# Optimization experiments

Measured on AMD Instinct MI355X. Metric: run time of the kernel, lower is better.

The kernel has to match this reference:

```python
import jax, jax.numpy as jnp
import numpy as np


def setup_inputs() -> dict:
    key = jax.random.key(0)
    k1, k2, k3 = jax.random.split(key, 3)
    N, K, d, d_out = 100000, 32, 64, 64
    x = jax.random.normal(k1, (N, d), dtype=jnp.float32)
    edge_index = jax.random.randint(k2, (N, K), 0, N, dtype=jnp.int64)
    W = jax.random.normal(k3, (2 * d, d_out), dtype=jnp.float32) * (1.0 / np.sqrt(2 * d))
    b = jnp.zeros((d_out,), dtype=jnp.float32)
    return {"x": x, "edge_index": edge_index, "W": W, "b": b}


def reference(x, edge_index, W, b):
    # x: [N, d], edge_index: [N, K] dense neighbor indices
    x_j = x[edge_index]                                  # [N, K, d] gather
    # concat([x_i, x_j - x_i]) then max over K. The x_i half is constant over K,
    # so its max is x itself; max of the diff half computed directly (same math,
    # avoids materializing the [N, K, 2d] concat).
    diff_max = jnp.max(x_j - x[:, None, :], axis=1)      # [N, d]
    h = jnp.concatenate([x, diff_max], axis=-1)          # [N, 2d]
    return h @ W + b                                     # [N, d_out]
```

## Files before the change

### kernel.cpp

```cpp
#include <hip/hip_runtime.h>
#include <hip/hip_bf16.h>
#include <cstdint>


typedef __attribute__((ext_vector_type(8))) short short8;
typedef __attribute__((ext_vector_type(4))) float f4;
typedef __attribute__((ext_vector_type(8))) unsigned short u16x8;
typedef __attribute__((ext_vector_type(4))) unsigned int u32x4;

#define TILE 16
#define ROWS 168

__device__ __forceinline__ unsigned short f2bf(float f) {
  unsigned int u = __builtin_bit_cast(unsigned int, f);
  u += 0x7fffu + ((u >> 16) & 1u);
  return (unsigned short)(u >> 16);
}
__device__ __forceinline__ unsigned int pack2(float a, float b) {
  return (unsigned int)f2bf(a) | ((unsigned int)f2bf(b) << 16);
}
__device__ __forceinline__ float bflo(unsigned int u) {
  return __builtin_bit_cast(float, u << 16);
}
__device__ __forceinline__ float bfhi(unsigned int u) {
  return __builtin_bit_cast(float, u & 0xffff0000u);
}
__device__ __forceinline__ unsigned int key2(unsigned int u) {
  unsigned int s = u & 0x80008000u;
  unsigned int m = (s >> 15) * 0x7fffu;
  return u ^ (0x80008000u | m);
}
__device__ __forceinline__ unsigned int unkey2(unsigned int k) {
  unsigned int s = k & 0x80008000u;
  unsigned int m = ((s >> 15) ^ 0x00010001u) * 0x7fffu;
  return k ^ (0x80008000u | m);
}
__device__ __forceinline__ u16x8 pmax8(u16x8 a, u16x8 b) {
  return __builtin_elementwise_max(a, b);
}

__global__ __launch_bounds__(256)
void convert_kernel(const float* __restrict__ x, unsigned int* __restrict__ xbf,
                    const float* __restrict__ W, unsigned short* __restrict__ wf,
                    int n8, int nxb) {
  if ((int)blockIdx.x < nxb) {
    int i = blockIdx.x * 256 + threadIdx.x;
    if (i >= n8) return;
    const f4* p = (const f4*)x + (size_t)i * 2;
    f4 a = __builtin_nontemporal_load(p);
    f4 b = __builtin_nontemporal_load(p + 1);
    u32x4 w;
    w.x = key2(pack2(a.x, a.y)); w.y = key2(pack2(a.z, a.w));
    w.z = key2(pack2(b.x, b.y)); w.w = key2(pack2(b.z, b.w));
    ((u32x4*)xbf)[i] = w;
  } else {
    #pragma unroll
    for (int q = 0; q < 4; ++q) {
      int idx = threadIdx.x * 4 + q;
      int wv = idx >> 8, ks = (idx >> 6) & 3, l = idx & 63;
      int c = l & 15, g = l >> 4;
      short8 v;
      #pragma unroll
      for (int j = 0; j < 8; ++j)
        v[j] = (short)f2bf(W[(ks * 32 + g * 8 + j) * 64 + wv * 16 + c]);
      *(short8*)(wf + (size_t)idx * 8) = v;
    }
  }
}

__global__ __launch_bounds__(256, 4)
void mrconv3_kernel(const unsigned int* __restrict__ xbf,
                    const unsigned short* __restrict__ wf,
                    const int* __restrict__ ei,
                    const float* __restrict__ bias,
                    float* __restrict__ out,
                    int n_tiles)
{
  __shared__ __align__(16) unsigned short hs[TILE * ROWS];
  __shared__ __align__(16) int eis[TILE * 32];
  __shared__ __align__(16) float otile[TILE * 64];

  const int tid  = threadIdx.x;
  const int wv   = tid >> 6;
  const int lane = tid & 63;
  const int c = lane & 15;
  const int g = lane >> 4;
  const int t2 = lane >> 4;
  const int h  = (lane >> 3) & 1;
  const int e  = lane & 7;

  const int node0 = blockIdx.x * TILE;
  const int t = wv * 4 + t2;

  {
    long long ev = __builtin_nontemporal_load(
        (const long long*)ei + (size_t)node0 * 16 + tid);
    const int ts = tid >> 4, qs = tid & 15;
    eis[ts * 32 + qs]      = (int)ev;
    eis[ts * 32 + 16 + qs] = (int)(ev >> 32);
  }
  __syncthreads();

  const char* __restrict__ xb = (const char*)xbf;
  const unsigned eoff = (unsigned)e * 16u;
  const u16x8 xrk = *(const u16x8*)(xb + ((unsigned)(node0 + t) * 128u + eoff));

  const int4* ip = (const int4*)&eis[(t * 2 + h) * 16];
  const int4 i0 = ip[0], i1 = ip[1], i2 = ip[2], i3 = ip[3];
  const int jj[16] = {i0.x, i0.y, i0.z, i0.w, i1.x, i1.y, i1.z, i1.w,
                      i2.x, i2.y, i2.z, i2.w, i3.x, i3.y, i3.z, i3.w};
  u16x8 r[16];
  #pragma unroll
  for (int q = 0; q < 16; ++q) {
    const unsigned vo = ((unsigned)jj[q] << 7) + eoff;
    asm volatile("global_load_dwordx4 %0, %1, %2"
                 : "=v"(r[q]) : "v"(vo), "s"(xbf));
  }
  asm volatile("s_waitcnt vmcnt(0)" ::: "memory");
  __builtin_amdgcn_sched_barrier(0);

  u16x8 ka = pmax8(r[0], r[1]);
  u16x8 kb = pmax8(r[2], r[3]);
  #pragma unroll
  for (int q = 4; q < 16; q += 4) {
    ka = pmax8(ka, pmax8(r[q],     r[q + 1]));
    kb = pmax8(kb, pmax8(r[q + 2], r[q + 3]));
  }
  u16x8 km = pmax8(ka, kb);

  u32x4 k4 = __builtin_bit_cast(u32x4, km);
  u32x4 s4;
  s4.x = (unsigned)__shfl_xor((int)k4.x, 8);
  s4.y = (unsigned)__shfl_xor((int)k4.y, 8);
  s4.z = (unsigned)__shfl_xor((int)k4.z, 8);
  s4.w = (unsigned)__shfl_xor((int)k4.w, 8);
  km = pmax8(km, __builtin_bit_cast(u16x8, s4));
  k4 = __builtin_bit_cast(u32x4, km);

  const u32x4 xr4 = __builtin_bit_cast(u32x4, xrk);
  u32x4 xw;
  xw.x = unkey2(xr4.x); xw.y = unkey2(xr4.y);
  xw.z = unkey2(xr4.z); xw.w = unkey2(xr4.w);

  if (h == 0) {
    const unsigned m0 = unkey2(k4.x), m1 = unkey2(k4.y);
    const unsigned m2 = unkey2(k4.z), m3 = unkey2(k4.w);
    u32x4 w;
    w.x = pack2(bflo(m0) - bflo(xw.x), bfhi(m0) - bfhi(xw.x));
    w.y = pack2(bflo(m1) - bflo(xw.y), bfhi(m1) - bfhi(xw.y));
    w.z = pack2(bflo(m2) - bflo(xw.z), bfhi(m2) - bfhi(xw.z));
    w.w = pack2(bflo(m3) - bflo(xw.w), bfhi(m3) - bfhi(xw.w));
    *(u32x4*)(hs + t * ROWS + 64 + e * 8) = w;
  } else {
    *(u32x4*)(hs + t * ROWS + e * 8) = xw;
  }

  short8 bfrag[4];
  #pragma unroll
  for (int ks = 0; ks < 4; ++ks)
    bfrag[ks] = *(const short8*)(wf + (size_t)((wv * 4 + ks) * 64 + lane) * 8);
  __syncthreads();

  f4 acc = {0.f, 0.f, 0.f, 0.f};
  #pragma unroll
  for (int ks = 0; ks < 4; ++ks) {
    short8 a = *(const short8*)(hs + c * ROWS + ks * 32 + g * 8);
    acc = __builtin_amdgcn_mfma_f32_16x16x32_bf16(a, bfrag[ks], acc, 0, 0, 0);
  }

  const float bb = bias[wv * 16 + c];
  #pragma unroll
  for (int j = 0; j < 4; ++j)
    otile[(g * 4 + j) * 64 + wv * 16 + c] = acc[j] + bb;
  __syncthreads();
  __builtin_nontemporal_store(*(const f4*)&otile[tid * 4],
                              (f4*)(out + (size_t)node0 * 64) + tid);
}

#define FWPB 4
#define FROWS 160
__global__ __launch_bounds__(256, 4)
void mrconv_fp32_kernel(const float* __restrict__ x,
                        const int* __restrict__ ei,
                        const float* __restrict__ W,
                        const float* __restrict__ bias,
                        float* __restrict__ out,
                        int n_tiles)
{
  __shared__ __align__(16) unsigned short hsf[FWPB][TILE * FROWS];
  const int wave = threadIdx.x >> 6;
  const int lane = threadIdx.x & 63;
  const int c = lane & 15;
  const int g = lane >> 4;

  short8 bfrag[4][4];
  #pragma unroll
  for (int ks = 0; ks < 4; ++ks) {
    #pragma unroll
    for (int nt = 0; nt < 4; ++nt) {
      short8 v;
      #pragma unroll
      for (int j = 0; j < 8; ++j) {
        int k = ks * 32 + g * 8 + j;
        v[j] = (short)f2bf(W[k * 64 + nt * 16 + c]);
      }
      bfrag[ks][nt] = v;
    }
  }

  const int tile = blockIdx.x * FWPB + wave;
  if (tile >= n_tiles) return;
  const int node0 = tile * TILE;
  unsigned short* hrow = &hsf[wave][0];

  #pragma unroll 2
  for (int t = 0; t < TILE; ++t) {
    const int n = node0 + t;
    const f4 xi = *(const f4*)(x + (size_t)n * 64 + 4 * c);
    f4 m = { -3.4e38f, -3.4e38f, -3.4e38f, -3.4e38f };
    #pragma unroll
    for (int it = 0; it < 8; ++it) {
      const int j = ei[(size_t)n * 32 + it * 4 + g];
      const f4 xj = *(const f4*)(x + (size_t)j * 64 + 4 * c);
      m.x = fmaxf(m.x, xj.x - xi.x);
      m.y = fmaxf(m.y, xj.y - xi.y);
      m.z = fmaxf(m.z, xj.z - xi.z);
      m.w = fmaxf(m.w, xj.w - xi.w);
    }
    m.x = fmaxf(m.x, __shfl_xor(m.x, 16));
    m.y = fmaxf(m.y, __shfl_xor(m.y, 16));
    m.z = fmaxf(m.z, __shfl_xor(m.z, 16));
    m.w = fmaxf(m.w, __shfl_xor(m.w, 16));
    m.x = fmaxf(m.x, __shfl_xor(m.x, 32));
    m.y = fmaxf(m.y, __shfl_xor(m.y, 32));
    m.z = fmaxf(m.z, __shfl_xor(m.z, 32));
    m.w = fmaxf(m.w, __shfl_xor(m.w, 32));
    if (g == 0) {
      ushort4 p;
      p.x = f2bf(xi.x); p.y = f2bf(xi.y); p.z = f2bf(xi.z); p.w = f2bf(xi.w);
      *(ushort4*)(hrow + t * FROWS + 4 * c) = p;
    } else if (g == 1) {
      ushort4 p;
      p.x = f2bf(m.x); p.y = f2bf(m.y); p.z = f2bf(m.z); p.w = f2bf(m.w);
      *(ushort4*)(hrow + t * FROWS + 64 + 4 * c) = p;
    }
  }
  __asm__ volatile("s_waitcnt lgkmcnt(0)" ::: "memory");

  f4 acc[4] = {{0.f,0.f,0.f,0.f},{0.f,0.f,0.f,0.f},{0.f,0.f,0.f,0.f},{0.f,0.f,0.f,0.f}};
  #pragma unroll
  for (int ks = 0; ks < 4; ++ks) {
    short8 a = *(const short8*)(hrow + c * FROWS + ks * 32 + g * 8);
    #pragma unroll
    for (int nt = 0; nt < 4; ++nt)
      acc[nt] = __builtin_amdgcn_mfma_f32_16x16x32_bf16(a, bfrag[ks][nt], acc[nt], 0, 0, 0);
  }
  const int rbase = node0 + g * 4;
  #pragma unroll
  for (int nt = 0; nt < 4; ++nt) {
    const float bb = bias[nt * 16 + c];
    #pragma unroll
    for (int j = 0; j < 4; ++j)
      out[(size_t)(rbase + j) * 64 + nt * 16 + c] = acc[nt][j] + bb;
  }
}

extern "C" void kernel_launch(void* const* d_in, const int* in_sizes, int n_in,
                              void* d_out, int out_size, void* d_ws, size_t ws_size,
                              hipStream_t stream) {
  const float* x  = (const float*)d_in[0];
  const int*   ei = (const int*)d_in[1];
  const float* W  = (const float*)d_in[2];
  const float* b  = (const float*)d_in[3];
  float* out = (float*)d_out;

  const int N = in_sizes[0] / 64;
  const int n_tiles = N / TILE;

  const size_t xbf_bytes = (size_t)N * 64 * 2;
  const size_t wf_bytes  = 1024 * 16;
  if (ws_size >= xbf_bytes + wf_bytes) {
    unsigned int*   xbf = (unsigned int*)d_ws;
    unsigned short* wf  = (unsigned short*)((char*)d_ws + xbf_bytes);
    const int n8  = N * 64 / 8;
    const int nxb = (n8 + 255) / 256;
    hipLaunchKernelGGL(convert_kernel, dim3(nxb + 1), dim3(256), 0, stream,
                       x, xbf, W, wf, n8, nxb);
    hipLaunchKernelGGL(mrconv3_kernel, dim3(n_tiles), dim3(256), 0, stream,
                       xbf, wf, ei, b, out, n_tiles);
  } else {
    const int blocks = (n_tiles + FWPB - 1) / FWPB;
    hipLaunchKernelGGL(mrconv_fp32_kernel, dim3(blocks), dim3(256), 0, stream,
                       x, ei, W, b, out, n_tiles);
  }
}
```

Before: 132.6 us.

## Stage neighbor gathers through LDS with double-buffered direct global-to-LDS loads

Replaces the 16 register-destined gather loads per lane with global_load_lds transfers into a per-wave double-buffered LDS staging area. The max reduction over one batch now overlaps with the in-flight loads of the next. It also reorders the edge-index layout in shared memory, hoists the weight fragment loads before the first barrier, and writes outputs straight to global instead of through an LDS tile and extra barrier. In exchange it uses more LDS per block, which may limit occupancy, and adds LDS round trips plus fine-grained waitcnt sequencing.

```diff
diff --git a/kernel.cpp b/kernel.cpp
--- a/kernel.cpp
+++ b/kernel.cpp
@@ -38,6 +38,18 @@
 __device__ __forceinline__ u16x8 pmax8(u16x8 a, u16x8 b) {
   return __builtin_elementwise_max(a, b);
 }
+__device__ __forceinline__ void gl16(const void* g, void* l) {
+  __builtin_amdgcn_global_load_lds(
+      (const __attribute__((address_space(1))) void*)g,
+      (__attribute__((address_space(3))) void*)l, 16, 0, 0);
+}
+
+#define WAITV4 do { asm volatile("s_waitcnt vmcnt(4)" ::: "memory"); \
+                    __builtin_amdgcn_sched_barrier(0); } while (0)
+#define WAITV0 do { asm volatile("s_waitcnt vmcnt(0)" ::: "memory"); \
+                    __builtin_amdgcn_sched_barrier(0); } while (0)
+#define WAITL0 do { asm volatile("s_waitcnt lgkmcnt(0)" ::: "memory"); \
+                    __builtin_amdgcn_sched_barrier(0); } while (0)
 
 __global__ __launch_bounds__(256)
 void convert_kernel(const float* __restrict__ x, unsigned int* __restrict__ xbf,
@@ -69,25 +81,26 @@
 }
 
 __global__ __launch_bounds__(256, 4)
-void mrconv3_kernel(const unsigned int* __restrict__ xbf,
+void mrconv4_kernel(const unsigned int* __restrict__ xbf,
                     const unsigned short* __restrict__ wf,
                     const int* __restrict__ ei,
                     const float* __restrict__ bias,
                     float* __restrict__ out,
                     int n_tiles)
 {
+  __shared__ __align__(16) unsigned short stg[4][2][2048];
+  __shared__ __align__(16) int eis3[512];
   __shared__ __align__(16) unsigned short hs[TILE * ROWS];
-  __shared__ __align__(16) int eis[TILE * 32];
-  __shared__ __align__(16) float otile[TILE * 64];
 
   const int tid  = threadIdx.x;
   const int wv   = tid >> 6;
   const int lane = tid & 63;
-  const int c = lane & 15;
-  const int g = lane >> 4;
+  const int c  = lane & 15;
+  const int g  = lane >> 4;
   const int t2 = lane >> 4;
-  const int h  = (lane >> 3) & 1;
+  const int rr = (lane >> 3) & 1;
   const int e  = lane & 7;
+  const int s  = lane >> 3;
 
   const int node0 = blockIdx.x * TILE;
   const int t = wv * 4 + t2;
@@ -96,36 +109,65 @@
     long long ev = __builtin_nontemporal_load(
         (const long long*)ei + (size_t)node0 * 16 + tid);
     const int ts = tid >> 4, qs = tid & 15;
-    eis[ts * 32 + qs]      = (int)ev;
-    eis[ts * 32 + 16 + qs] = (int)(ev >> 32);
-  }
+    const int k0 = qs * 2, k1 = qs * 2 + 1;
+    eis3[((k0 & 7) * 16 + ts) * 4 + (k0 >> 3)] = (int)ev;
+    eis3[((k1 & 7) * 16 + ts) * 4 + (k1 >> 3)] = (int)(ev >> 32);
+  }
+
+  const char* __restrict__ xb = (const char*)xbf;
+  const unsigned co = (unsigned)e * 16u;
+  const u16x8 xrk = *(const u16x8*)(xb + (size_t)((unsigned)(node0 + t) * 128u + co));
+  short8 bfrag[4];
+  #pragma unroll
+  for (int ks = 0; ks < 4; ++ks)
+    bfrag[ks] = *(const short8*)(wf + (size_t)((wv * 4 + ks) * 64 + lane) * 8);
   __syncthreads();
 
-  const char* __restrict__ xb = (const char*)xbf;
-  const unsigned eoff = (unsigned)e * 16u;
-  const u16x8 xrk = *(const u16x8*)(xb + ((unsigned)(node0 + t) * 128u + eoff));
-
-  const int4* ip = (const int4*)&eis[(t * 2 + h) * 16];
-  const int4 i0 = ip[0], i1 = ip[1], i2 = ip[2], i3 = ip[3];
-  const int jj[16] = {i0.x, i0.y, i0.z, i0.w, i1.x, i1.y, i1.z, i1.w,
-                      i2.x, i2.y, i2.z, i2.w, i3.x, i3.y, i3.z, i3.w};
-  u16x8 r[16];
-  #pragma unroll
-  for (int q = 0; q < 16; ++q) {
-    const unsigned vo = ((unsigned)jj[q] << 7) + eoff;
-    asm volatile("global_load_dwordx4 %0, %1, %2"
-                 : "=v"(r[q]) : "v"(vo), "s"(xbf));
-  }
-  asm volatile("s_waitcnt vmcnt(0)" ::: "memory");
-  __builtin_amdgcn_sched_barrier(0);
-
-  u16x8 ka = pmax8(r[0], r[1]);
-  u16x8 kb = pmax8(r[2], r[3]);
-  #pragma unroll
-  for (int q = 4; q < 16; q += 4) {
-    ka = pmax8(ka, pmax8(r[q],     r[q + 1]));
-    kb = pmax8(kb, pmax8(r[q + 2], r[q + 3]));
-  }
+  const int4 q0 = *(const int4*)&eis3[(s * 16 + wv * 4 + 0) * 4];
+  const int4 q1 = *(const int4*)&eis3[(s * 16 + wv * 4 + 1) * 4];
+  const int4 q2 = *(const int4*)&eis3[(s * 16 + wv * 4 + 2) * 4];
+  const int4 q3 = *(const int4*)&eis3[(s * 16 + wv * 4 + 3) * 4];
+
+  unsigned short* const sw0 = &stg[wv][0][0];
+  unsigned short* const sw1 = &stg[wv][1][0];
+
+#define ISS(I0, I1, I2, I3, SW)                                   \
+  gl16(xb + ((unsigned)(I0) * 128u + co), (SW));                  \
+  gl16(xb + ((unsigned)(I1) * 128u + co), (SW) + 512);            \
+  gl16(xb + ((unsigned)(I2) * 128u + co), (SW) + 1024);           \
+  gl16(xb + ((unsigned)(I3) * 128u + co), (SW) + 1536)
+
+  const unsigned rbase = (unsigned)t2 * 512 + (unsigned)rr * 256 + (unsigned)e * 8;
+
+  u16x8 ka, kb;
+#define RED_INIT(SW) {                                            \
+    const u16x8 v0 = *(const u16x8*)((SW) + rbase);               \
+    const u16x8 v1 = *(const u16x8*)((SW) + rbase + 64);          \
+    const u16x8 v2 = *(const u16x8*)((SW) + rbase + 128);         \
+    const u16x8 v3 = *(const u16x8*)((SW) + rbase + 192);         \
+    ka = pmax8(v0, v2); kb = pmax8(v1, v3); }
+#define RED_ACC(SW) {                                             \
+    const u16x8 v0 = *(const u16x8*)((SW) + rbase);               \
+    const u16x8 v1 = *(const u16x8*)((SW) + rbase + 64);          \
+    const u16x8 v2 = *(const u16x8*)((SW) + rbase + 128);         \
+    const u16x8 v3 = *(const u16x8*)((SW) + rbase + 192);         \
+    ka = pmax8(ka, pmax8(v0, v2)); kb = pmax8(kb, pmax8(v1, v3)); }
+
+  ISS(q0.x, q1.x, q2.x, q3.x, sw0);
+  ISS(q0.y, q1.y, q2.y, q3.y, sw1);
+  WAITV4;
+  RED_INIT(sw0);
+  WAITL0;
+  ISS(q0.z, q1.z, q2.z, q3.z, sw0);
+  WAITV4;
+  RED_ACC(sw1);
+  WAITL0;
+  ISS(q0.w, q1.w, q2.w, q3.w, sw1);
+  WAITV4;
+  RED_ACC(sw0);
+  WAITV0;
+  RED_ACC(sw1);
+
   u16x8 km = pmax8(ka, kb);
 
   u32x4 k4 = __builtin_bit_cast(u32x4, km);
@@ -142,7 +184,7 @@
   xw.x = unkey2(xr4.x); xw.y = unkey2(xr4.y);
   xw.z = unkey2(xr4.z); xw.w = unkey2(xr4.w);
 
-  if (h == 0) {
+  if (rr == 0) {
     const unsigned m0 = unkey2(k4.x), m1 = unkey2(k4.y);
     const unsigned m2 = unkey2(k4.z), m3 = unkey2(k4.w);
     u32x4 w;
@@ -154,11 +196,6 @@
   } else {
     *(u32x4*)(hs + t * ROWS + e * 8) = xw;
   }
-
-  short8 bfrag[4];
-  #pragma unroll
-  for (int ks = 0; ks < 4; ++ks)
-    bfrag[ks] = *(const short8*)(wf + (size_t)((wv * 4 + ks) * 64 + lane) * 8);
   __syncthreads();
 
   f4 acc = {0.f, 0.f, 0.f, 0.f};
@@ -171,10 +208,11 @@
   const float bb = bias[wv * 16 + c];
   #pragma unroll
   for (int j = 0; j < 4; ++j)
-    otile[(g * 4 + j) * 64 + wv * 16 + c] = acc[j] + bb;
-  __syncthreads();
-  __builtin_nontemporal_store(*(const f4*)&otile[tid * 4],
-                              (f4*)(out + (size_t)node0 * 64) + tid);
+    __builtin_nontemporal_store(acc[j] + bb,
+        out + (size_t)(node0 + g * 4 + j) * 64 + wv * 16 + c);
+#undef ISS
+#undef RED_INIT
+#undef RED_ACC
 }
 
 #define FWPB 4
@@ -286,7 +324,7 @@
     const int nxb = (n8 + 255) / 256;
     hipLaunchKernelGGL(convert_kernel, dim3(nxb + 1), dim3(256), 0, stream,
                        x, xbf, W, wf, n8, nxb);
-    hipLaunchKernelGGL(mrconv3_kernel, dim3(n_tiles), dim3(256), 0, stream,
+    hipLaunchKernelGGL(mrconv4_kernel, dim3(n_tiles), dim3(256), 0, stream,
                        xbf, wf, ei, b, out, n_tiles);
   } else {
     const int blocks = (n_tiles + FWPB - 1) / FWPB;
```

Result: no change. 134.6 us (+1.5%).
